# Kernel tuning notes

Measured on AMD Instinct MI355X. Metric: run time of the kernel, lower is better.

The kernel has to match this reference:

```python
import jax, jax.numpy as jnp
import numpy as np

NEG_BIG = -9e15
ALPHA = 0.2  # LeakyReLU negative slope


def setup_inputs() -> dict:
    key = jax.random.key(0)
    k1, k2, k3, k4 = jax.random.split(key, 4)
    N, Fin, Fout = 8192, 256, 256
    input_ = jax.random.normal(k1, (N, Fin), dtype=jnp.float32)
    adj = jax.random.randint(k2, (N, N), 0, 2, dtype=jnp.int32)
    # xavier_uniform with gain=1.414
    limW = 1.414 * np.sqrt(6.0 / (Fin + Fout))
    W = jax.random.uniform(k3, (Fin, Fout), minval=-limW, maxval=limW, dtype=jnp.float32)
    lima = 1.414 * np.sqrt(6.0 / (2 * Fout + 1))
    a = jax.random.uniform(k4, (2 * Fout, 1), minval=-lima, maxval=lima, dtype=jnp.float32)
    return {"input_": input_, "adj": adj, "W": W, "a": a}


def reference(input_, adj, W, a):
    # h: [N, F]
    h = input_ @ W
    F = h.shape[1]
    # Decompose cat([h_i, h_j]) @ a into per-node projections summed by broadcast
    src = h @ a[:F, 0]   # [N]  contribution of row node i
    dst = h @ a[F:, 0]   # [N]  contribution of col node j
    e = jax.nn.leaky_relu(src[:, None] + dst[None, :], negative_slope=ALPHA)  # [N, N]
    e = jnp.where(adj > 0, e, NEG_BIG)
    attention = jax.nn.softmax(e, axis=1)
    h_prime = attention @ h  # [N, F]
    return jax.nn.relu(h_prime)  # concat=True
```

## Files before the change

kernel.cpp:

```cpp
#include <hip/hip_runtime.h>
#include <math.h>

#define NN 8192
#define FF 256
#define ALPHA 0.2f
#define SS 4
#define JSEG (NN / SS)
#define STEPS (JSEG / 32)

typedef __bf16 bf16x8 __attribute__((ext_vector_type(8)));
typedef __bf16 bf16x4 __attribute__((ext_vector_type(4)));
typedef float  f32x4  __attribute__((ext_vector_type(4)));

__device__ __forceinline__ void dma16(const void* g, void* l) {
    __builtin_amdgcn_global_load_lds((const __attribute__((address_space(1))) void*)g,
                                     (__attribute__((address_space(3))) void*)l,
                                     16, 0, 0);
}

__global__ __launch_bounds__(256) void k0_wt(const float* __restrict__ W,
                                             __bf16* __restrict__ WT) {
    __shared__ float ts[64][65];
    const int t = threadIdx.x;
    const int k0 = blockIdx.x * 64;
    const int n0 = blockIdx.y * 64;
    #pragma unroll
    for (int r = 0; r < 4; ++r) {
        int krow = r * 16 + (t >> 4);
        int nc4 = (t & 15) * 4;
        *(float4*)&ts[krow][nc4] = *(const float4*)&W[(size_t)(k0 + krow) * FF + n0 + nc4];
    }
    __syncthreads();
    const int nloc = t >> 2;
    const int kc = (t & 3) * 16;
    union { bf16x8 v[2]; __bf16 e[16]; } hi, lo;
    #pragma unroll
    for (int u = 0; u < 16; ++u) {
        float x = ts[kc + u][nloc];
        __bf16 h1 = (__bf16)x;
        hi.e[u] = h1;
        lo.e[u] = (__bf16)(x - (float)h1);
    }
    size_t base = (size_t)(n0 + nloc) * FF + k0 + kc;
    *(bf16x8*)&WT[base] = hi.v[0];
    *(bf16x8*)&WT[base + 8] = hi.v[1];
    size_t lbase = (size_t)FF * FF + base;
    *(bf16x8*)&WT[lbase] = lo.v[0];
    *(bf16x8*)&WT[lbase + 8] = lo.v[1];
}

__global__ __launch_bounds__(256) void k1_h(const float* __restrict__ X,
                                            const __bf16* __restrict__ WT,
                                            const float* __restrict__ a,
                                            __bf16* __restrict__ hT,
                                            float* __restrict__ src,
                                            float* __restrict__ dst) {
    __shared__ __bf16 ax[2][32][40];
    __shared__ float hs[32][264];
    __shared__ float red[2][4][32];
    const int t = threadIdx.x;
    const int i0 = blockIdx.x * 32;
    const int l = t & 63, wv = t >> 6, ln = l & 15, g = l >> 4;
    f32x4 acc[2][4];
    #pragma unroll
    for (int mt = 0; mt < 2; ++mt)
        #pragma unroll
        for (int nt = 0; nt < 4; ++nt)
            acc[mt][nt] = (f32x4){0.f, 0.f, 0.f, 0.f};

    for (int ks = 0; ks < 8; ++ks) {
        const int k0 = ks * 32;
        {
            int row = t >> 3, c4 = (t & 7) * 4;
            float4 xv = *(const float4*)&X[(size_t)(i0 + row) * FF + k0 + c4];
            bf16x4 hi4, lo4;
            float xs_[4] = {xv.x, xv.y, xv.z, xv.w};
            #pragma unroll
            for (int u = 0; u < 4; ++u) {
                __bf16 h1 = (__bf16)xs_[u];
                hi4[u] = h1;
                lo4[u] = (__bf16)(xs_[u] - (float)h1);
            }
            *(bf16x4*)&ax[0][row][c4] = hi4;
            *(bf16x4*)&ax[1][row][c4] = lo4;
        }
        __syncthreads();
        bf16x8 ah[2], al[2];
        ah[0] = *(bf16x8*)&ax[0][ln][g * 8];
        ah[1] = *(bf16x8*)&ax[0][16 + ln][g * 8];
        al[0] = *(bf16x8*)&ax[1][ln][g * 8];
        al[1] = *(bf16x8*)&ax[1][16 + ln][g * 8];
        #pragma unroll
        for (int nt = 0; nt < 4; ++nt) {
            const int n = wv * 64 + nt * 16 + ln;
            bf16x8 bh8 = *(const bf16x8*)&WT[(size_t)n * FF + k0 + g * 8];
            bf16x8 bl8 = *(const bf16x8*)&WT[(size_t)(FF + n) * FF + k0 + g * 8];
            #pragma unroll
            for (int mt = 0; mt < 2; ++mt) {
                acc[mt][nt] = __builtin_amdgcn_mfma_f32_16x16x32_bf16(ah[mt], bh8, acc[mt][nt], 0, 0, 0);
                acc[mt][nt] = __builtin_amdgcn_mfma_f32_16x16x32_bf16(ah[mt], bl8, acc[mt][nt], 0, 0, 0);
                acc[mt][nt] = __builtin_amdgcn_mfma_f32_16x16x32_bf16(al[mt], bh8, acc[mt][nt], 0, 0, 0);
            }
        }
        __syncthreads();
    }
    float an[4], ad[4];
    #pragma unroll
    for (int nt = 0; nt < 4; ++nt) {
        an[nt] = a[wv * 64 + nt * 16 + ln];
        ad[nt] = a[FF + wv * 64 + nt * 16 + ln];
    }
    float sp[2][4], dp[2][4];
    #pragma unroll
    for (int mt = 0; mt < 2; ++mt)
        #pragma unroll
        for (int rg = 0; rg < 4; ++rg) { sp[mt][rg] = 0.f; dp[mt][rg] = 0.f; }
    #pragma unroll
    for (int mt = 0; mt < 2; ++mt)
        #pragma unroll
        for (int nt = 0; nt < 4; ++nt)
            #pragma unroll
            for (int rg = 0; rg < 4; ++rg) {
                float v = acc[mt][nt][rg];
                hs[mt * 16 + g * 4 + rg][wv * 64 + nt * 16 + ln] = v;
                sp[mt][rg] += v * an[nt];
                dp[mt][rg] += v * ad[nt];
            }
    #pragma unroll
    for (int mk = 1; mk < 16; mk <<= 1)
        #pragma unroll
        for (int mt = 0; mt < 2; ++mt)
            #pragma unroll
            for (int rg = 0; rg < 4; ++rg) {
                sp[mt][rg] += __shfl_xor(sp[mt][rg], mk);
                dp[mt][rg] += __shfl_xor(dp[mt][rg], mk);
            }
    if (ln == 0) {
        #pragma unroll
        for (int mt = 0; mt < 2; ++mt)
            #pragma unroll
            for (int rg = 0; rg < 4; ++rg) {
                red[0][wv][mt * 16 + g * 4 + rg] = sp[mt][rg];
                red[1][wv][mt * 16 + g * 4 + rg] = dp[mt][rg];
            }
    }
    __syncthreads();
    if (t < 32) {
        src[i0 + t] = red[0][0][t] + red[0][1][t] + red[0][2][t] + red[0][3][t];
        dst[i0 + t] = red[1][0][t] + red[1][1][t] + red[1][2][t] + red[1][3][t];
    }
    {
        const int f = t;
        #pragma unroll
        for (int jc = 0; jc < 4; ++jc) {
            union { bf16x8 v; __bf16 e[8]; } hi, lo;
            #pragma unroll
            for (int u = 0; u < 8; ++u) {
                float x = hs[jc * 8 + u][f];
                __bf16 h1 = (__bf16)x;
                hi.e[u] = h1;
                lo.e[u] = (__bf16)(x - (float)h1);
            }
            *(bf16x8*)&hT[(size_t)f * NN + i0 + jc * 8] = hi.v;
            *(bf16x8*)&hT[(size_t)(FF + f) * NN + i0 + jc * 8] = lo.v;
        }
    }
}

__global__ __launch_bounds__(256) void k2b_max(const float* __restrict__ dst,
                                               float* __restrict__ maxd) {
    __shared__ float red[256];
    float m = -1e30f;
    #pragma unroll
    for (int r = 0; r < NN / 1024; ++r) {
        float4 v = *(const float4*)&dst[(r * 256 + threadIdx.x) * 4];
        m = fmaxf(m, fmaxf(fmaxf(v.x, v.y), fmaxf(v.z, v.w)));
    }
    red[threadIdx.x] = m;
    __syncthreads();
    for (int s = 128; s > 0; s >>= 1) {
        if (threadIdx.x < s) red[threadIdx.x] = fmaxf(red[threadIdx.x], red[threadIdx.x + s]);
        __syncthreads();
    }
    if (threadIdx.x == 0) maxd[0] = red[0];
}

__global__ __launch_bounds__(256, 2) void k3_attn(const int* __restrict__ adj,
                                                  const __bf16* __restrict__ hT,
                                                  const float* __restrict__ src,
                                                  const float* __restrict__ dst,
                                                  const float* __restrict__ maxd,
                                                  float* __restrict__ num,
                                                  float* __restrict__ den) {
    __shared__ __bf16 bh[2][2048 * 8];
    __shared__ __bf16 wA[2][64][40];
    __shared__ float dl[64][4];
    const int t = threadIdx.x;
    const int l = t & 63, wv = t >> 6, ln = l & 15, g = l >> 4;
    const int it = blockIdx.x & 127;
    const int seg = blockIdx.x >> 7;
    const int i0 = it * 64;
    const int jbeg = seg * JSEG;
    const int p_i = t >> 2, p_q = t & 3;
    const float maxdv = maxd[0];
    const float src_r = src[i0 + p_i];
    const float e0 = src_r + maxdv;
    const float m_r = e0 > 0.f ? e0 : ALPHA * e0;

    int rowbase[8], cb[8];
    #pragma unroll
    for (int r = 0; r < 8; ++r) {
        int cbase = r * 256 + wv * 64;
        int c = cbase + l;
        int hl = c >> 10;
        int f = (c >> 2) & 255;
        int pc = c & 3;
        int jc = pc ^ ((f >> 1) & 3);
        rowbase[r] = (hl * FF + f) * NN + jc * 8;
        cb[r] = __builtin_amdgcn_readfirstlane(cbase);
    }
    const int* arow = adj + (size_t)(i0 + p_i) * NN + p_q * 8;

    #pragma unroll
    for (int r = 0; r < 8; ++r)
        dma16(&hT[rowbase[r] + jbeg], &bh[0][cb[r] * 8]);
    int4 a0 = *(const int4*)(arow + jbeg);
    int4 a1 = *(const int4*)(arow + jbeg + 4);
    float4 d0 = *(const float4*)&dst[jbeg + p_q * 8];
    float4 d1 = *(const float4*)&dst[jbeg + p_q * 8 + 4];

    float den_reg = 0.f;
    f32x4 acc[4][4];
    #pragma unroll
    for (int mt = 0; mt < 4; ++mt)
        #pragma unroll
        for (int nt = 0; nt < 4; ++nt)
            acc[mt][nt] = (f32x4){0.f, 0.f, 0.f, 0.f};

    for (int s = 0; s < STEPS; ++s) {
        const int cur = s & 1;
        {
            const int av[8] = {a0.x, a0.y, a0.z, a0.w, a1.x, a1.y, a1.z, a1.w};
            const float dv[8] = {d0.x, d0.y, d0.z, d0.w, d1.x, d1.y, d1.z, d1.w};
            union { bf16x8 v; __bf16 e[8]; } wu;
            #pragma unroll
            for (int u = 0; u < 8; ++u) {
                float e = src_r + dv[u];
                e = e > 0.f ? e : ALPHA * e;
                float w = (av[u] > 0) ? __expf(e - m_r) : 0.f;
                den_reg += w;
                wu.e[u] = (__bf16)w;
            }
            *(bf16x8*)&wA[cur][p_i][p_q * 8] = wu.v;
        }
        __syncthreads();
        if (s + 1 < STEPS) {
            const int j1 = jbeg + (s + 1) * 32;
            #pragma unroll
            for (int r = 0; r < 8; ++r)
                dma16(&hT[rowbase[r] + j1], &bh[cur ^ 1][cb[r] * 8]);
            a0 = *(const int4*)(arow + j1);
            a1 = *(const int4*)(arow + j1 + 4);
            d0 = *(const float4*)&dst[j1 + p_q * 8];
            d1 = *(const float4*)&dst[j1 + p_q * 8 + 4];
        }
        bf16x8 af[4];
        #pragma unroll
        for (int mt = 0; mt < 4; ++mt)
            af[mt] = *(bf16x8*)&wA[cur][mt * 16 + ln][g * 8];
        #pragma unroll
        for (int nt = 0; nt < 4; ++nt) {
            const int f = wv * 64 + nt * 16 + ln;
            const int sw = (f >> 1) & 3;
            #pragma unroll
            for (int hl = 0; hl < 2; ++hl) {
                const int chunk = (hl * FF + f) * 4 + (g ^ sw);
                bf16x8 bfr = *(bf16x8*)&bh[cur][chunk * 8];
                #pragma unroll
                for (int mt = 0; mt < 4; ++mt)
                    acc[mt][nt] = __builtin_amdgcn_mfma_f32_16x16x32_bf16(
                        af[mt], bfr, acc[mt][nt], 0, 0, 0);
            }
        }
    }
    #pragma unroll
    for (int mt = 0; mt < 4; ++mt)
        #pragma unroll
        for (int nt = 0; nt < 4; ++nt)
            #pragma unroll
            for (int rg = 0; rg < 4; ++rg)
                num[((size_t)seg * NN + i0 + mt * 16 + g * 4 + rg) * FF
                    + wv * 64 + nt * 16 + ln] = acc[mt][nt][rg];
    dl[p_i][p_q] = den_reg;
    __syncthreads();
    if (t < 64) den[(size_t)seg * NN + i0 + t] = dl[t][0] + dl[t][1] + dl[t][2] + dl[t][3];
}

__global__ __launch_bounds__(256) void k4_out(const float* __restrict__ num,
                                              const float* __restrict__ den,
                                              float* __restrict__ out) {
    size_t f4 = (size_t)blockIdx.x * 256 + threadIdx.x;
    int i = (int)(f4 >> 6);
    int c4 = (int)(f4 & 63) << 2;
    float4 s = make_float4(0.f, 0.f, 0.f, 0.f);
    float d = 0.f;
    #pragma unroll
    for (int sg = 0; sg < SS; ++sg) {
        float4 v = *(const float4*)&num[((size_t)sg * NN + i) * FF + c4];
        s.x += v.x; s.y += v.y; s.z += v.z; s.w += v.w;
        d += den[(size_t)sg * NN + i];
    }
    float inv = 1.f / d;
    float4 o;
    o.x = fmaxf(s.x * inv, 0.f);
    o.y = fmaxf(s.y * inv, 0.f);
    o.z = fmaxf(s.z * inv, 0.f);
    o.w = fmaxf(s.w * inv, 0.f);
    *(float4*)&out[(size_t)i * FF + c4] = o;
}

extern "C" void kernel_launch(void* const* d_in, const int* in_sizes, int n_in,
                              void* d_out, int out_size, void* d_ws, size_t ws_size,
                              hipStream_t stream) {
    const float* X  = (const float*)d_in[0];
    const int*  adj = (const int*)d_in[1];
    const float* W  = (const float*)d_in[2];
    const float* a  = (const float*)d_in[3];
    float* out = (float*)d_out;
    char* ws = (char*)d_ws;

    const size_t off_hT   = 0;
    const size_t off_wt   = off_hT + (size_t)2 * FF * NN * 2;
    const size_t off_src  = off_wt + (size_t)2 * FF * FF * 2;
    const size_t off_dst  = off_src + (size_t)NN * 4;
    const size_t off_maxd = off_dst + (size_t)NN * 4;
    const size_t off_num  = off_maxd + 256;
    const size_t off_den  = off_num + (size_t)SS * NN * FF * 4;

    __bf16* hT_ws = (__bf16*)(ws + off_hT);
    __bf16* wt_ws = (__bf16*)(ws + off_wt);
    float* src_ws = (float*)(ws + off_src);
    float* dst_ws = (float*)(ws + off_dst);
    float* maxd   = (float*)(ws + off_maxd);
    float* num_ws = (float*)(ws + off_num);
    float* den_ws = (float*)(ws + off_den);

    k0_wt<<<dim3(FF / 64, FF / 64), 256, 0, stream>>>(W, wt_ws);
    k1_h<<<NN / 32, 256, 0, stream>>>(X, wt_ws, a, hT_ws, src_ws, dst_ws);
    k2b_max<<<1, 256, 0, stream>>>(dst_ws, maxd);
    k3_attn<<<(NN / 64) * SS, 256, 0, stream>>>(adj, hT_ws, src_ws, dst_ws, maxd,
                                                num_ws, den_ws);
    k4_out<<<(NN * FF / 4) / 256, 256, 0, stream>>>(num_ws, den_ws, out);
}
```

Before: 481.9 us.

## Prefetch adj/dst two steps ahead and replace syncthreads with targeted waitcnt barrier

The adjacency and dst loads become register double-buffered and are issued two steps ahead of use, so their global latency can hide behind a full iteration of MFMA work. The generic __syncthreads is replaced by explicit s_waitcnt vmcnt(4), lgkmcnt(0) and s_barrier. This lets the four just-issued prefetch loads stay in flight across the barrier, while the LDS DMA for the current tile is still forced to complete. In exchange, correctness now depends on hand-counted vmcnt ordering and compiler fences. The final steps also issue redundant loads and DMA at jbeg, and the extra prefetch registers raise register pressure.

```diff
diff --git a/kernel.cpp b/kernel.cpp
--- a/kernel.cpp
+++ b/kernel.cpp
@@ -17,6 +17,11 @@
                                      (__attribute__((address_space(3))) void*)l,
                                      16, 0, 0);
 }
+
+#define VMCNT4   asm volatile("s_waitcnt vmcnt(4)" ::: "memory")
+#define LGKM0    asm volatile("s_waitcnt lgkmcnt(0)" ::: "memory")
+#define BARRIER  asm volatile("s_barrier" ::: "memory")
+#define FENCE    asm volatile("" ::: "memory")
 
 __global__ __launch_bounds__(256) void k0_wt(const float* __restrict__ W,
                                              __bf16* __restrict__ WT) {
@@ -221,13 +226,21 @@
     }
     const int* arow = adj + (size_t)(i0 + p_i) * NN + p_q * 8;
 
+    int4 A0[2], A1[2];
+    float4 D0[2], D1[2];
+    A0[0] = *(const int4*)(arow + jbeg);
+    A1[0] = *(const int4*)(arow + jbeg + 4);
+    D0[0] = *(const float4*)&dst[jbeg + p_q * 8];
+    D1[0] = *(const float4*)&dst[jbeg + p_q * 8 + 4];
+    FENCE;
     #pragma unroll
     for (int r = 0; r < 8; ++r)
         dma16(&hT[rowbase[r] + jbeg], &bh[0][cb[r] * 8]);
-    int4 a0 = *(const int4*)(arow + jbeg);
-    int4 a1 = *(const int4*)(arow + jbeg + 4);
-    float4 d0 = *(const float4*)&dst[jbeg + p_q * 8];
-    float4 d1 = *(const float4*)&dst[jbeg + p_q * 8 + 4];
+    FENCE;
+    A0[1] = *(const int4*)(arow + jbeg + 32);
+    A1[1] = *(const int4*)(arow + jbeg + 32 + 4);
+    D0[1] = *(const float4*)&dst[jbeg + 32 + p_q * 8];
+    D1[1] = *(const float4*)&dst[jbeg + 32 + p_q * 8 + 4];
 
     float den_reg = 0.f;
     f32x4 acc[4][4];
@@ -238,10 +251,12 @@
             acc[mt][nt] = (f32x4){0.f, 0.f, 0.f, 0.f};
 
     for (int s = 0; s < STEPS; ++s) {
-        const int cur = s & 1;
+        const int p = s & 1;
         {
-            const int av[8] = {a0.x, a0.y, a0.z, a0.w, a1.x, a1.y, a1.z, a1.w};
-            const float dv[8] = {d0.x, d0.y, d0.z, d0.w, d1.x, d1.y, d1.z, d1.w};
+            const int av[8] = {A0[p].x, A0[p].y, A0[p].z, A0[p].w,
+                               A1[p].x, A1[p].y, A1[p].z, A1[p].w};
+            const float dv[8] = {D0[p].x, D0[p].y, D0[p].z, D0[p].w,
+                                 D1[p].x, D1[p].y, D1[p].z, D1[p].w};
             union { bf16x8 v; __bf16 e[8]; } wu;
             #pragma unroll
             for (int u = 0; u < 8; ++u) {
@@ -251,23 +266,29 @@
                 den_reg += w;
                 wu.e[u] = (__bf16)w;
             }
-            *(bf16x8*)&wA[cur][p_i][p_q * 8] = wu.v;
-        }
-        __syncthreads();
-        if (s + 1 < STEPS) {
-            const int j1 = jbeg + (s + 1) * 32;
+            *(bf16x8*)&wA[p][p_i][p_q * 8] = wu.v;
+        }
+        {
+            const int jn = (s + 2 < STEPS) ? jbeg + (s + 2) * 32 : jbeg;
+            A0[p] = *(const int4*)(arow + jn);
+            A1[p] = *(const int4*)(arow + jn + 4);
+            D0[p] = *(const float4*)&dst[jn + p_q * 8];
+            D1[p] = *(const float4*)&dst[jn + p_q * 8 + 4];
+        }
+        VMCNT4;
+        LGKM0;
+        BARRIER;
+        {
+            const int j1 = (s + 1 < STEPS) ? jbeg + (s + 1) * 32 : jbeg;
             #pragma unroll
             for (int r = 0; r < 8; ++r)
-                dma16(&hT[rowbase[r] + j1], &bh[cur ^ 1][cb[r] * 8]);
-            a0 = *(const int4*)(arow + j1);
-            a1 = *(const int4*)(arow + j1 + 4);
-            d0 = *(const float4*)&dst[j1 + p_q * 8];
-            d1 = *(const float4*)&dst[j1 + p_q * 8 + 4];
-        }
+                dma16(&hT[rowbase[r] + j1], &bh[p ^ 1][cb[r] * 8]);
+        }
+        FENCE;
         bf16x8 af[4];
         #pragma unroll
         for (int mt = 0; mt < 4; ++mt)
-            af[mt] = *(bf16x8*)&wA[cur][mt * 16 + ln][g * 8];
+            af[mt] = *(bf16x8*)&wA[p][mt * 16 + ln][g * 8];
         #pragma unroll
         for (int nt = 0; nt < 4; ++nt) {
             const int f = wv * 64 + nt * 16 + ln;
@@ -275,7 +296,7 @@
             #pragma unroll
             for (int hl = 0; hl < 2; ++hl) {
                 const int chunk = (hl * FF + f) * 4 + (g ^ sw);
-                bf16x8 bfr = *(bf16x8*)&bh[cur][chunk * 8];
+                bf16x8 bfr = *(bf16x8*)&bh[p][chunk * 8];
                 #pragma unroll
                 for (int mt = 0; mt < 4; ++mt)
                     acc[mt][nt] = __builtin_amdgcn_mfma_f32_16x16x32_bf16(
```

Measured after the change: 639.6 us. 32.7% more time.

## Unroll attention loop by two with deeper adj/dst prefetch and manual waitcnts

Applied to the files above, without the earlier changes.

Restructures the main attention-times-h loop into a two-step unrolled pipeline. Adjacency and dst loads are prefetched two steps ahead in separate even/odd register sets, and the compiler's conservative syncthreads is replaced by explicit s_waitcnt vmcnt(4)/lgkmcnt(0) plus s_barrier. The goal is to keep global loads in flight across barriers so load latency overlaps with MFMA work. It relies on hand-counted outstanding memory operations, which could be wrong if the compiler reorders loads, and it issues redundant prefetches at the tail.

```diff
diff --git a/kernel.cpp b/kernel.cpp
--- a/kernel.cpp
+++ b/kernel.cpp
@@ -17,6 +17,11 @@
                                      (__attribute__((address_space(3))) void*)l,
                                      16, 0, 0);
 }
+
+#define VMCNT4   asm volatile("s_waitcnt vmcnt(4)" ::: "memory")
+#define LGKM0    asm volatile("s_waitcnt lgkmcnt(0)" ::: "memory")
+#define BARRIER  asm volatile("s_barrier" ::: "memory")
+#define FENCE    asm volatile("" ::: "memory")
 
 __global__ __launch_bounds__(256) void k0_wt(const float* __restrict__ W,
                                              __bf16* __restrict__ WT) {
@@ -220,14 +225,25 @@
         cb[r] = __builtin_amdgcn_readfirstlane(cbase);
     }
     const int* arow = adj + (size_t)(i0 + p_i) * NN + p_q * 8;
-
+    const float* drow = dst + p_q * 8;
+
+    int4 a0e, a1e, a0o, a1o;
+    float4 d0e, d1e, d0o, d1o;
+
+    a0e = *(const int4*)(arow + jbeg);
+    a1e = *(const int4*)(arow + jbeg + 4);
+    d0e = *(const float4*)(drow + jbeg);
+    d1e = *(const float4*)(drow + jbeg + 4);
+    FENCE;
     #pragma unroll
     for (int r = 0; r < 8; ++r)
         dma16(&hT[rowbase[r] + jbeg], &bh[0][cb[r] * 8]);
-    int4 a0 = *(const int4*)(arow + jbeg);
-    int4 a1 = *(const int4*)(arow + jbeg + 4);
-    float4 d0 = *(const float4*)&dst[jbeg + p_q * 8];
-    float4 d1 = *(const float4*)&dst[jbeg + p_q * 8 + 4];
+    FENCE;
+    a0o = *(const int4*)(arow + jbeg + 32);
+    a1o = *(const int4*)(arow + jbeg + 32 + 4);
+    d0o = *(const float4*)(drow + jbeg + 32);
+    d1o = *(const float4*)(drow + jbeg + 32 + 4);
+    FENCE;
 
     float den_reg = 0.f;
     f32x4 acc[4][4];
@@ -237,52 +253,83 @@
         for (int nt = 0; nt < 4; ++nt)
             acc[mt][nt] = (f32x4){0.f, 0.f, 0.f, 0.f};
 
-    for (int s = 0; s < STEPS; ++s) {
-        const int cur = s & 1;
+#define K3_WCOMP(A0_, A1_, D0_, D1_, P_)                                      \
+    {                                                                         \
+        const int av[8] = {A0_.x, A0_.y, A0_.z, A0_.w,                        \
+                           A1_.x, A1_.y, A1_.z, A1_.w};                       \
+        const float dv[8] = {D0_.x, D0_.y, D0_.z, D0_.w,                      \
+                             D1_.x, D1_.y, D1_.z, D1_.w};                     \
+        union { bf16x8 v; __bf16 e[8]; } wu;                                  \
+        _Pragma("unroll")                                                     \
+        for (int u = 0; u < 8; ++u) {                                         \
+            float e = src_r + dv[u];                                          \
+            e = e > 0.f ? e : ALPHA * e;                                      \
+            float w = (av[u] > 0) ? __expf(e - m_r) : 0.f;                    \
+            den_reg += w;                                                     \
+            wu.e[u] = (__bf16)w;                                              \
+        }                                                                     \
+        *(bf16x8*)&wA[P_][p_i][p_q * 8] = wu.v;                               \
+    }
+
+#define K3_PREF(A0_, A1_, D0_, D1_, JN_)                                      \
+    A0_ = *(const int4*)(arow + (JN_));                                       \
+    A1_ = *(const int4*)(arow + (JN_) + 4);                                   \
+    D0_ = *(const float4*)(drow + (JN_));                                     \
+    D1_ = *(const float4*)(drow + (JN_) + 4);
+
+#define K3_DMA(J1_, P_)                                                       \
+    {                                                                         \
+        _Pragma("unroll")                                                     \
+        for (int r = 0; r < 8; ++r)                                           \
+            dma16(&hT[rowbase[r] + (J1_)], &bh[P_][cb[r] * 8]);               \
+    }
+
+#define K3_MFMA(P_)                                                           \
+    {                                                                         \
+        bf16x8 af[4];                                                         \
+        _Pragma("unroll")                                                     \
+        for (int mt = 0; mt < 4; ++mt)                                        \
+            af[mt] = *(bf16x8*)&wA[P_][mt * 16 + ln][g * 8];                  \
+        _Pragma("unroll")                                                     \
+        for (int nt = 0; nt < 4; ++nt) {                                      \
+            const int f = wv * 64 + nt * 16 + ln;                             \
+            const int sw = (f >> 1) & 3;                                      \
+            _Pragma("unroll")                                                 \
+            for (int hl = 0; hl < 2; ++hl) {                                  \
+                const int chunk = (hl * FF + f) * 4 + (g ^ sw);               \
+                bf16x8 bfr = *(bf16x8*)&bh[P_][chunk * 8];                    \
+                _Pragma("unroll")                                             \
+                for (int mt = 0; mt < 4; ++mt)                                \
+                    acc[mt][nt] = __builtin_amdgcn_mfma_f32_16x16x32_bf16(    \
+                        af[mt], bfr, acc[mt][nt], 0, 0, 0);                   \
+            }                                                                 \
+        }                                                                     \
+    }
+
+    for (int su = 0; su < STEPS; su += 2) {
+        K3_WCOMP(a0e, a1e, d0e, d1e, 0);
         {
-            const int av[8] = {a0.x, a0.y, a0.z, a0.w, a1.x, a1.y, a1.z, a1.w};
-            const float dv[8] = {d0.x, d0.y, d0.z, d0.w, d1.x, d1.y, d1.z, d1.w};
-            union { bf16x8 v; __bf16 e[8]; } wu;
-            #pragma unroll
-            for (int u = 0; u < 8; ++u) {
-                float e = src_r + dv[u];
-                e = e > 0.f ? e : ALPHA * e;
-                float w = (av[u] > 0) ? __expf(e - m_r) : 0.f;
-                den_reg += w;
-                wu.e[u] = (__bf16)w;
-            }
-            *(bf16x8*)&wA[cur][p_i][p_q * 8] = wu.v;
-        }
-        __syncthreads();
-        if (s + 1 < STEPS) {
-            const int j1 = jbeg + (s + 1) * 32;
-            #pragma unroll
-            for (int r = 0; r < 8; ++r)
-                dma16(&hT[rowbase[r] + j1], &bh[cur ^ 1][cb[r] * 8]);
-            a0 = *(const int4*)(arow + j1);
-            a1 = *(const int4*)(arow + j1 + 4);
-            d0 = *(const float4*)&dst[j1 + p_q * 8];
-            d1 = *(const float4*)&dst[j1 + p_q * 8 + 4];
-        }
-        bf16x8 af[4];
-        #pragma unroll
-        for (int mt = 0; mt < 4; ++mt)
-            af[mt] = *(bf16x8*)&wA[cur][mt * 16 + ln][g * 8];
-        #pragma unroll
-        for (int nt = 0; nt < 4; ++nt) {
-            const int f = wv * 64 + nt * 16 + ln;
-            const int sw = (f >> 1) & 3;
-            #pragma unroll
-            for (int hl = 0; hl < 2; ++hl) {
-                const int chunk = (hl * FF + f) * 4 + (g ^ sw);
-                bf16x8 bfr = *(bf16x8*)&bh[cur][chunk * 8];
-                #pragma unroll
-                for (int mt = 0; mt < 4; ++mt)
-                    acc[mt][nt] = __builtin_amdgcn_mfma_f32_16x16x32_bf16(
-                        af[mt], bfr, acc[mt][nt], 0, 0, 0);
-            }
-        }
-    }
+            const int jn = (su + 2 < STEPS) ? jbeg + (su + 2) * 32 : jbeg;
+            K3_PREF(a0e, a1e, d0e, d1e, jn);
+        }
+        FENCE; VMCNT4; LGKM0; BARRIER;
+        K3_DMA(jbeg + (su + 1) * 32, 1);
+        FENCE;
+        K3_MFMA(0);
+        K3_WCOMP(a0o, a1o, d0o, d1o, 1);
+        {
+            const int jn = (su + 3 < STEPS) ? jbeg + (su + 3) * 32 : jbeg;
+            K3_PREF(a0o, a1o, d0o, d1o, jn);
+        }
+        FENCE; VMCNT4; LGKM0; BARRIER;
+        {
+            const int j2 = (su + 2 < STEPS) ? jbeg + (su + 2) * 32 : jbeg;
+            K3_DMA(j2, 0);
+        }
+        FENCE;
+        K3_MFMA(1);
+    }
+    __syncthreads();
     #pragma unroll
     for (int mt = 0; mt < 4; ++mt)
         #pragma unroll
```

Measured after the change: 486.0 us. No clear change (+0.8%).
